# Optimization experiments

Hardware: AMD Instinct MI355X
Metric: run time of the kernel (lower is better)

The kernel has to match this reference:

```python
import jax, jax.numpy as jnp
import numpy as np


def setup_inputs() -> dict:
    key = jax.random.key(0)
    k1, k2, k3 = jax.random.split(key, 3)
    V, B, T = 8192, 8, 1024
    x = jax.random.randint(k1, (B, T), 0, V, dtype=jnp.int64)
    y = jax.random.randint(k2, (B, T), 0, V, dtype=jnp.int64)
    emb = jax.random.normal(k3, (V, V), dtype=jnp.float32)
    return {"x": x, "y": y, "emb": emb}


def reference(x, y, emb):
    # token embedding lookup: [B, T, C] with C == vocab_size
    logits = emb[x]
    B, T, C = logits.shape
    # Causal mean pooling. softmax over a tril(ones) mask assigns uniform
    # weight 1/(t+1) to positions 0..t, i.e. a causal running mean.
    # Equivalent to the original's avg_matrix @ logits, computed in O(T*C).
    denom = jnp.arange(1, T + 1, dtype=logits.dtype)[:, None]  # [T, 1]
    logits_prev_mean = jnp.cumsum(logits, axis=1) / denom      # [B, T, C]
    # cross_entropy with mean reduction over B*T positions
    logp = jax.nn.log_softmax(logits_prev_mean, axis=-1)
    nll = -jnp.take_along_axis(logp, y[..., None], axis=-1)[..., 0]  # [B, T]
    loss = jnp.mean(nll)
    return logits, loss
```

## Files before the change

### kernel.cpp

```cpp
#include <hip/hip_runtime.h>

#define V 8192
#define B 8
#define T 1024
#define NSEG 16
#define SEGLEN 64
#define CSLICE 1024
#define NCHUNK 32
#define CHUNK 256

__global__ __launch_bounds__(256) void sum_kernel(
    const float* __restrict__ emb, const int* __restrict__ x,
    float* __restrict__ segsum)
{
    const int slice = blockIdx.x;
    const int seg   = blockIdx.y;
    const int b     = blockIdx.z;
    const int c4    = (slice * CSLICE + threadIdx.x * 4) >> 2;

    const float4* emb4 = (const float4*)emb;
    float4 acc = make_float4(0.f, 0.f, 0.f, 0.f);
#pragma unroll 4
    for (int i = 0; i < SEGLEN; ++i) {
        const int row = x[b * T + seg * SEGLEN + i];
        float4 v = emb4[(size_t)row * (V / 4) + c4];
        acc.x += v.x; acc.y += v.y; acc.z += v.z; acc.w += v.w;
    }
    ((float4*)segsum)[(size_t)(b * NSEG + seg) * (V / 4) + c4] = acc;
}

__global__ __launch_bounds__(256) void fused_kernel(
    const float* __restrict__ emb, const int* __restrict__ x,
    const int* __restrict__ y, const float* __restrict__ segsum,
    float* __restrict__ logits, float* __restrict__ P, float* __restrict__ tval)
{
    const int wave  = threadIdx.x >> 6;
    const int lane  = threadIdx.x & 63;
    const int chunk = blockIdx.x * 4 + wave;
    const int seg   = blockIdx.y;
    const int b     = blockIdx.z;
    const int c0    = chunk * CHUNK + lane * 4;
    const int c4    = c0 >> 2;

    const float4* ss4 = (const float4*)segsum;
    float4 S = make_float4(0.f, 0.f, 0.f, 0.f);
    for (int s = 0; s < seg; ++s) {
        float4 v = ss4[(size_t)(b * NSEG + s) * (V / 4) + c4];
        S.x += v.x; S.y += v.y; S.z += v.z; S.w += v.w;
    }

    const float4* emb4    = (const float4*)emb;
    float4*       logits4 = (float4*)logits;
    for (int i = 0; i < SEGLEN; ++i) {
        const int t   = seg * SEGLEN + i;
        const int pos = b * T + t;
        const int row = x[pos];
        float4 v = emb4[(size_t)row * (V / 4) + c4];
        logits4[(size_t)pos * (V / 4) + c4] = v;
        S.x += v.x; S.y += v.y; S.z += v.z; S.w += v.w;
        const float inv = 1.0f / (float)(t + 1);
        const float m0 = S.x * inv, m1 = S.y * inv, m2 = S.z * inv, m3 = S.w * inv;
        float e = __expf(m0) + __expf(m1) + __expf(m2) + __expf(m3);

        const int yc = y[pos];
        const unsigned d = (unsigned)(yc - c0);
        if (d < 4u) {
            const float mv = (d == 0) ? m0 : (d == 1) ? m1 : (d == 2) ? m2 : m3;
            tval[pos] = mv;
        }
#pragma unroll
        for (int off = 32; off; off >>= 1) e += __shfl_xor(e, off, 64);
        if (lane == 0) P[(size_t)chunk * (B * T) + pos] = e;
    }
}

__global__ __launch_bounds__(256) void loss_kernel(
    const float* __restrict__ P, const float* __restrict__ tval,
    float* __restrict__ loss)
{
    const int pos = blockIdx.x * 256 + threadIdx.x;
    float s = 0.f;
#pragma unroll
    for (int ch = 0; ch < NCHUNK; ++ch) s += P[(size_t)ch * (B * T) + pos];
    float nll = __logf(s) - tval[pos];

#pragma unroll
    for (int off = 32; off; off >>= 1) nll += __shfl_xor(nll, off, 64);
    __shared__ float red[4];
    const int wid = threadIdx.x >> 6;
    if ((threadIdx.x & 63) == 0) red[wid] = nll;
    __syncthreads();
    if (threadIdx.x == 0) {
        const float tot = red[0] + red[1] + red[2] + red[3];
        atomicAdd(loss, tot * (1.0f / (float)(B * T)));
    }
}

extern "C" void kernel_launch(void* const* d_in, const int* in_sizes, int n_in,
                              void* d_out, int out_size, void* d_ws, size_t ws_size,
                              hipStream_t stream) {
    const int*   x   = (const int*)d_in[0];
    const int*   y   = (const int*)d_in[1];
    const float* emb = (const float*)d_in[2];

    float* logits = (float*)d_out;
    float* loss   = logits + (size_t)B * T * V;

    float* segsum = (float*)d_ws;
    float* P      = segsum + (size_t)B * NSEG * V;
    float* tval   = P + (size_t)NCHUNK * B * T;

    hipMemsetAsync(loss, 0, sizeof(float), stream);
    sum_kernel<<<dim3(V / CSLICE, NSEG, B), 256, 0, stream>>>(emb, x, segsum);
    fused_kernel<<<dim3(NCHUNK / 4, NSEG, B), 256, 0, stream>>>(emb, x, y, segsum, logits, P, tval);
    loss_kernel<<<dim3(B * T / 256), 256, 0, stream>>>(P, tval, loss);
}
```

Baseline: 484.9 us.

## Prefetch embedding rows with register double-buffering and batch index loads via shuffles

Both the segment-sum and fused kernels now load the token and target indices once per wave, one per lane, and broadcast them with shuffles instead of issuing a scalar load each iteration. Embedding row loads are software-pipelined four iterations ahead in a register buffer to hide gather latency. Logits are written with nontemporal stores, and the per-position partial sums are collected into one lane each and written as a single coalesced store at the end. The cost is more registers and extra shuffle instructions per iteration.

```diff
diff --git a/kernel.cpp b/kernel.cpp
--- a/kernel.cpp
+++ b/kernel.cpp
@@ -9,6 +9,12 @@
 #define NCHUNK 32
 #define CHUNK 256
 
+typedef float f32x4 __attribute__((ext_vector_type(4)));
+
+__device__ __forceinline__ void nt_store4(float4* p, float4 v) {
+    __builtin_nontemporal_store(*(f32x4*)&v, (f32x4*)p);
+}
+
 __global__ __launch_bounds__(256) void sum_kernel(
     const float* __restrict__ emb, const int* __restrict__ x,
     float* __restrict__ segsum)
@@ -16,15 +22,28 @@
     const int slice = blockIdx.x;
     const int seg   = blockIdx.y;
     const int b     = blockIdx.z;
+    const int lane  = threadIdx.x & 63;
     const int c4    = (slice * CSLICE + threadIdx.x * 4) >> 2;
+
+    const int xi = x[b * T + seg * SEGLEN + lane];
 
     const float4* emb4 = (const float4*)emb;
     float4 acc = make_float4(0.f, 0.f, 0.f, 0.f);
-#pragma unroll 4
-    for (int i = 0; i < SEGLEN; ++i) {
-        const int row = x[b * T + seg * SEGLEN + i];
-        float4 v = emb4[(size_t)row * (V / 4) + c4];
-        acc.x += v.x; acc.y += v.y; acc.z += v.z; acc.w += v.w;
+    float4 vbuf[4];
+#pragma unroll
+    for (int k = 0; k < 4; ++k)
+        vbuf[k] = emb4[(size_t)__shfl(xi, k, 64) * (V / 4) + c4];
+
+#pragma unroll
+    for (int i = 0; i < SEGLEN; i += 4) {
+#pragma unroll
+        for (int k = 0; k < 4; ++k) {
+            float4 cur = vbuf[k];
+            const int nxt = i + 4 + k;
+            if (nxt < SEGLEN)
+                vbuf[k] = emb4[(size_t)__shfl(xi, nxt, 64) * (V / 4) + c4];
+            acc.x += cur.x; acc.y += cur.y; acc.z += cur.z; acc.w += cur.w;
+        }
     }
     ((float4*)segsum)[(size_t)(b * NSEG + seg) * (V / 4) + c4] = acc;
 }
@@ -41,6 +60,7 @@
     const int b     = blockIdx.z;
     const int c0    = chunk * CHUNK + lane * 4;
     const int c4    = c0 >> 2;
+    const int tbase = seg * SEGLEN;
 
     const float4* ss4 = (const float4*)segsum;
     float4 S = make_float4(0.f, 0.f, 0.f, 0.f);
@@ -49,29 +69,48 @@
         S.x += v.x; S.y += v.y; S.z += v.z; S.w += v.w;
     }
 
+    const int   xi   = x[b * T + tbase + lane];
+    const int   yi   = y[b * T + tbase + lane];
+    const float invi = 1.0f / (float)(tbase + lane + 1);
+
     const float4* emb4    = (const float4*)emb;
     float4*       logits4 = (float4*)logits;
-    for (int i = 0; i < SEGLEN; ++i) {
-        const int t   = seg * SEGLEN + i;
-        const int pos = b * T + t;
-        const int row = x[pos];
-        float4 v = emb4[(size_t)row * (V / 4) + c4];
-        logits4[(size_t)pos * (V / 4) + c4] = v;
-        S.x += v.x; S.y += v.y; S.z += v.z; S.w += v.w;
-        const float inv = 1.0f / (float)(t + 1);
-        const float m0 = S.x * inv, m1 = S.y * inv, m2 = S.z * inv, m3 = S.w * inv;
-        float e = __expf(m0) + __expf(m1) + __expf(m2) + __expf(m3);
 
-        const int yc = y[pos];
-        const unsigned d = (unsigned)(yc - c0);
-        if (d < 4u) {
-            const float mv = (d == 0) ? m0 : (d == 1) ? m1 : (d == 2) ? m2 : m3;
-            tval[pos] = mv;
+    float4 vbuf[4];
+#pragma unroll
+    for (int k = 0; k < 4; ++k)
+        vbuf[k] = emb4[(size_t)__shfl(xi, k, 64) * (V / 4) + c4];
+
+    float myP = 0.f;
+    for (int i = 0; i < SEGLEN; i += 4) {
+#pragma unroll
+        for (int k = 0; k < 4; ++k) {
+            const int ii  = i + k;
+            float4 cur = vbuf[k];
+            const int nxt = ii + 4;
+            if (nxt < SEGLEN)
+                vbuf[k] = emb4[(size_t)__shfl(xi, nxt, 64) * (V / 4) + c4];
+
+            const int t   = tbase + ii;
+            const int pos = b * T + t;
+            nt_store4(&logits4[(size_t)pos * (V / 4) + c4], cur);
+            S.x += cur.x; S.y += cur.y; S.z += cur.z; S.w += cur.w;
+            const float inv = __shfl(invi, ii, 64);
+            const float m0 = S.x * inv, m1 = S.y * inv, m2 = S.z * inv, m3 = S.w * inv;
+            float e = __expf(m0) + __expf(m1) + __expf(m2) + __expf(m3);
+
+            const int yc = __shfl(yi, ii, 64);
+            const unsigned d = (unsigned)(yc - c0);
+            if (d < 4u) {
+                const float mv = (d == 0) ? m0 : (d == 1) ? m1 : (d == 2) ? m2 : m3;
+                tval[pos] = mv;
+            }
+#pragma unroll
+            for (int off = 32; off; off >>= 1) e += __shfl_xor(e, off, 64);
+            if (lane == ii) myP = e;
         }
-#pragma unroll
-        for (int off = 32; off; off >>= 1) e += __shfl_xor(e, off, 64);
-        if (lane == 0) P[(size_t)chunk * (B * T) + pos] = e;
     }
+    P[(size_t)chunk * (B * T) + b * T + tbase + lane] = myP;
 }
 
 __global__ __launch_bounds__(256) void loss_kernel(
```

After: 468.0 us. 1.04x faster.
